# Performance work log

Measured on AMD Instinct MI355X. Metric: run time of the kernel, lower is better.

The kernel has to match this reference:

```python
import jax, jax.numpy as jnp
import numpy as np

B = 1048576


def _normalize_rotation_matrix(R):
    # Faithful to torch: U, S, V = svd(R); Rn = U @ V^T; flip whole U by sign(det); recompute.
    U, S, Vh = jnp.linalg.svd(R)  # R = U diag(S) Vh, so torch's V^T == Vh
    Rn = jnp.matmul(U, Vh)
    det = jnp.linalg.det(Rn)[:, None, None]
    sign = jnp.sign(det)
    U = U * sign
    return jnp.matmul(U, Vh)


def _quat_to_rotmat(q):
    # q: [B, 4] as (w, x, y, z); same element layout as the torch loop, vectorized.
    w, x, y, z = q[:, 0], q[:, 1], q[:, 2], q[:, 3]
    R = jnp.stack([
        1 - 2 * (y ** 2 + z ** 2), 2 * (x * y - w * z),     2 * (x * z + w * y),
        2 * (x * y + w * z),       1 - 2 * (x ** 2 + z ** 2), 2 * (y * z - w * x),
        2 * (x * z - w * y),       2 * (y * z + w * x),     1 - 2 * (x ** 2 + y ** 2),
    ], axis=-1)
    return R.reshape(-1, 3, 3)


def setup_inputs() -> dict:
    key = jax.random.key(0)
    k1, k2, k3 = jax.random.split(key, 3)
    pred_R = jax.random.normal(k1, (B, 3, 3), dtype=jnp.float32)
    pred_t = jax.random.normal(k2, (B, 1, 3), dtype=jnp.float32)
    gt_transform = jax.random.normal(k3, (B, 7), dtype=jnp.float32)
    return {"pred_R": pred_R, "pred_t": pred_t, "gt_transform": gt_transform}


def reference(pred_R, pred_t, gt_transform):
    gt_quat = gt_transform[:, :4]
    igt_t = gt_transform[:, 4:]
    igt_R = _quat_to_rotmat(gt_quat)              # [B,3,3]
    igt_R = _normalize_rotation_matrix(igt_R)
    pred_Rn = _normalize_rotation_matrix(pred_R)
    # matmul(pred_R^T, igt_R): [b,i,k] = sum_j pred_Rn[b,j,i] * igt_R[b,j,k]
    M = jnp.einsum('bji,bjk->bik', pred_Rn, igt_R)
    eye = jnp.eye(3, dtype=M.dtype)
    rot_loss = jnp.mean((M - eye) ** 2)
    t_loss = jnp.mean((pred_t - igt_t[:, None, :]) ** 2)
    return rot_loss + t_loss
```

## Files before the change

kernel.cpp:

```cpp
#include <hip/hip_runtime.h>


#define TILE 256
#define SCALED_ITERS 3
#define PLAIN_ITERS  1

__device__ __forceinline__ float se3_elem(const float* __restrict__ R,
                                          const float* __restrict__ Q,
                                          const float* __restrict__ T)
{
    float w  = Q[0], x = Q[1], y = Q[2], z = Q[3];

    float v2 = x*x + y*y + z*z;
    float c  = 1.0f - 2.0f*v2;
    float r2 = fmaxf(c*c + 4.0f*(w*w)*v2, 1e-30f);
    float rr = __builtin_amdgcn_rsqf(r2);
    float ga = c * rr;
    float gt_ = (1.0f - ga) * __builtin_amdgcn_rcpf(fmaxf(v2, 1e-37f));
    float gb = 2.0f * w * rr;

    float tx = gt_*x, ty = gt_*y, tz = gt_*z;
    float bx = gb*x,  by = gb*y,  bz = gb*z;

    float G0 = ga + tx*x,  G1 = tx*y - bz,   G2 = tx*z + by;
    float G3 = tx*y + bz,  G4 = ga + ty*y,   G5 = ty*z - bx;
    float G6 = tx*z - by,  G7 = ty*z + bx,   G8 = ga + tz*z;

    float X0 = R[0], X1 = R[1], X2 = R[2];
    float X3 = R[3], X4 = R[4], X5 = R[5];
    float X6 = R[6], X7 = R[7], X8 = R[8];

    float s = 1.0f;
#pragma unroll
    for (int it = 0; it < SCALED_ITERS + PLAIN_ITERS; ++it) {
        float C0 = X4*X8 - X5*X7;
        float C1 = X5*X6 - X3*X8;
        float C2 = X3*X7 - X4*X6;
        float C3 = X2*X7 - X1*X8;
        float C4 = X0*X8 - X2*X6;
        float C5 = X1*X6 - X0*X7;
        float C6 = X1*X5 - X2*X4;
        float C7 = X2*X3 - X0*X5;
        float C8 = X0*X4 - X1*X3;
        float det = X0*C0 + X1*C1 + X2*C2;
        if (it == 0) s = (det < 0.0f) ? -1.0f : 1.0f;
        float ka, kb;
        if (it < SCALED_ITERS) {
            float ad = fminf(fmaxf(fabsf(det), 1e-30f), 1e30f);
            float g  = __builtin_amdgcn_exp2f(0.33333333f * __builtin_amdgcn_logf(ad));
            ka = 0.5f * __builtin_amdgcn_rcpf(g);
            kb = 0.5f * g * __builtin_amdgcn_rcpf(det);
        } else {
            ka = 0.5f;
            kb = 0.5f * __builtin_amdgcn_rcpf(det);
        }
        if (it == SCALED_ITERS + PLAIN_ITERS - 1) { ka *= s; kb *= s; }
        X0 = ka*X0 + kb*C0;  X1 = ka*X1 + kb*C1;  X2 = ka*X2 + kb*C2;
        X3 = ka*X3 + kb*C3;  X4 = ka*X4 + kb*C4;  X5 = ka*X5 + kb*C5;
        X6 = ka*X6 + kb*C6;  X7 = ka*X7 + kb*C7;  X8 = ka*X8 + kb*C8;
    }

    float d0 = G0-X0, d1 = G1-X1, d2 = G2-X2;
    float d3 = G3-X3, d4 = G4-X4, d5 = G5-X5;
    float d6 = G6-X6, d7 = G7-X7, d8 = G8-X8;
    float rot = d0*d0 + d1*d1 + d2*d2
              + d3*d3 + d4*d4 + d5*d5
              + d6*d6 + d7*d7 + d8*d8;

    float e0 = T[0] - Q[4];
    float e1 = T[1] - Q[5];
    float e2 = T[2] - Q[6];
    float tl = e0*e0 + e1*e1 + e2*e2;

    return rot * (1.0f/9.0f) + tl * (1.0f/3.0f);
}

__device__ __forceinline__ float se3_block_partial(
    const float* __restrict__ pred_R,
    const float* __restrict__ pred_t,
    const float* __restrict__ gt,
    int B, float invB,
    float* ldsR, float* ldsQ, float* ldsT, float* wsums)
{
    const int tid  = threadIdx.x;
    const int base = blockIdx.x * TILE;
    int count = B - base;
    if (count > TILE) count = TILE;

    if (count == TILE) {
        const float4* sR = reinterpret_cast<const float4*>(pred_R) + (size_t)blockIdx.x * (TILE * 9 / 4);
        const float4* sQ = reinterpret_cast<const float4*>(gt)     + (size_t)blockIdx.x * (TILE * 7 / 4);
        const float4* sT = reinterpret_cast<const float4*>(pred_t) + (size_t)blockIdx.x * (TILE * 3 / 4);
        float4* dR = reinterpret_cast<float4*>(ldsR);
        float4* dQ = reinterpret_cast<float4*>(ldsQ);
        float4* dT = reinterpret_cast<float4*>(ldsT);

        float4 r0 = sR[tid];
        float4 r1 = sR[tid + 256];
        float4 r2; if (tid < 64)  r2 = sR[tid + 512];
        float4 q0 = sQ[tid];
        float4 q1; if (tid < 192) q1 = sQ[tid + 256];
        float4 t0; if (tid < 192) t0 = sT[tid];

        dR[tid]       = r0;
        dR[tid + 256] = r1;
        if (tid < 64)  dR[tid + 512] = r2;
        dQ[tid]       = q0;
        if (tid < 192) dQ[tid + 256] = q1;
        if (tid < 192) dT[tid]       = t0;
    } else {
        for (int i = tid; i < count * 9; i += 256) ldsR[i] = pred_R[(size_t)base * 9 + i];
        for (int i = tid; i < count * 7; i += 256) ldsQ[i] = gt[(size_t)base * 7 + i];
        for (int i = tid; i < count * 3; i += 256) ldsT[i] = pred_t[(size_t)base * 3 + i];
    }
    __syncthreads();

    float acc = 0.0f;
    if (tid < count)
        acc = se3_elem(&ldsR[9 * tid], &ldsQ[7 * tid], &ldsT[3 * tid]) * invB;

#pragma unroll
    for (int off = 32; off > 0; off >>= 1)
        acc += __shfl_down(acc, off, 64);

    int lane = tid & 63;
    int wid  = tid >> 6;
    if (lane == 0) wsums[wid] = acc;
    __syncthreads();
    return wsums[0] + wsums[1] + wsums[2] + wsums[3];
}

__global__ __launch_bounds__(256) void se3_partial_kernel(
    const float* __restrict__ pred_R,
    const float* __restrict__ pred_t,
    const float* __restrict__ gt,
    float* __restrict__ partials, int B, float invB)
{
    __shared__ __align__(16) float ldsR[TILE * 9];
    __shared__ __align__(16) float ldsQ[TILE * 7];
    __shared__ __align__(16) float ldsT[TILE * 3];
    __shared__ float wsums[4];

    float tot = se3_block_partial(pred_R, pred_t, gt, B, invB,
                                  ldsR, ldsQ, ldsT, wsums);
    if (threadIdx.x == 0)
        partials[blockIdx.x] = tot;
}

__global__ __launch_bounds__(256) void se3_atomic_kernel(
    const float* __restrict__ pred_R,
    const float* __restrict__ pred_t,
    const float* __restrict__ gt,
    float* __restrict__ out, int B, float invB)
{
    __shared__ __align__(16) float ldsR[TILE * 9];
    __shared__ __align__(16) float ldsQ[TILE * 7];
    __shared__ __align__(16) float ldsT[TILE * 3];
    __shared__ float wsums[4];

    float tot = se3_block_partial(pred_R, pred_t, gt, B, invB,
                                  ldsR, ldsQ, ldsT, wsums);
    if (threadIdx.x == 0)
        atomicAdd(out, tot);
}

__global__ __launch_bounds__(256) void se3_reduce_kernel(
    const float* __restrict__ partials, float* __restrict__ out, int n)
{
    float acc = 0.0f;
    for (int i = threadIdx.x; i < n; i += 256)
        acc += partials[i];

#pragma unroll
    for (int off = 32; off > 0; off >>= 1)
        acc += __shfl_down(acc, off, 64);

    __shared__ float wsums[4];
    int lane = threadIdx.x & 63;
    int wid  = threadIdx.x >> 6;
    if (lane == 0) wsums[wid] = acc;
    __syncthreads();
    if (threadIdx.x == 0)
        out[0] = wsums[0] + wsums[1] + wsums[2] + wsums[3];
}

extern "C" void kernel_launch(void* const* d_in, const int* in_sizes, int n_in,
                              void* d_out, int out_size, void* d_ws, size_t ws_size,
                              hipStream_t stream) {
    const float* pred_R = (const float*)d_in[0];
    const float* pred_t = (const float*)d_in[1];
    const float* gt     = (const float*)d_in[2];
    float* out = (float*)d_out;
    int B = in_sizes[0] / 9;

    const int block = 256;
    const int grid  = (B + TILE - 1) / TILE;

    if (d_ws != nullptr && ws_size >= (size_t)grid * sizeof(float)) {
        float* partials = (float*)d_ws;
        se3_partial_kernel<<<grid, block, 0, stream>>>(pred_R, pred_t, gt,
                                                       partials, B,
                                                       1.0f / (float)B);
        se3_reduce_kernel<<<1, block, 0, stream>>>(partials, out, grid);
    } else {
        hipMemsetAsync(out, 0, sizeof(float), stream);
        se3_atomic_kernel<<<grid, block, 0, stream>>>(pred_R, pred_t, gt,
                                                      out, B, 1.0f / (float)B);
    }
}
```

Baseline: 106.6 us.

## Process four tiles per block with double-buffered LDS and register prefetch

Each block of the partial kernel now handles four consecutive 256-element tiles. While it computes on one LDS buffer, it prefetches the next tile into registers and then stores it into the alternate buffer. The grid shrinks by four, so the partials array and the final reduction get smaller, and global load latency overlaps with the heavy per-element math. In exchange, LDS use per block doubles, which can lower occupancy, and extra barriers are added per tile.

```diff
diff --git a/kernel.cpp b/kernel.cpp
--- a/kernel.cpp
+++ b/kernel.cpp
@@ -2,6 +2,7 @@
 
 
 #define TILE 256
+#define TPB_TILES 4
 #define SCALED_ITERS 3
 #define PLAIN_ITERS  1
 
@@ -75,76 +76,114 @@
     return rot * (1.0f/9.0f) + tl * (1.0f/3.0f);
 }
 
-__device__ __forceinline__ float se3_block_partial(
-    const float* __restrict__ pred_R,
-    const float* __restrict__ pred_t,
-    const float* __restrict__ gt,
-    int B, float invB,
-    float* ldsR, float* ldsQ, float* ldsT, float* wsums)
-{
-    const int tid  = threadIdx.x;
-    const int base = blockIdx.x * TILE;
-    int count = B - base;
-    if (count > TILE) count = TILE;
-
-    if (count == TILE) {
-        const float4* sR = reinterpret_cast<const float4*>(pred_R) + (size_t)blockIdx.x * (TILE * 9 / 4);
-        const float4* sQ = reinterpret_cast<const float4*>(gt)     + (size_t)blockIdx.x * (TILE * 7 / 4);
-        const float4* sT = reinterpret_cast<const float4*>(pred_t) + (size_t)blockIdx.x * (TILE * 3 / 4);
-        float4* dR = reinterpret_cast<float4*>(ldsR);
-        float4* dQ = reinterpret_cast<float4*>(ldsQ);
-        float4* dT = reinterpret_cast<float4*>(ldsT);
-
-        float4 r0 = sR[tid];
-        float4 r1 = sR[tid + 256];
-        float4 r2; if (tid < 64)  r2 = sR[tid + 512];
-        float4 q0 = sQ[tid];
-        float4 q1; if (tid < 192) q1 = sQ[tid + 256];
-        float4 t0; if (tid < 192) t0 = sT[tid];
-
-        dR[tid]       = r0;
-        dR[tid + 256] = r1;
-        if (tid < 64)  dR[tid + 512] = r2;
-        dQ[tid]       = q0;
-        if (tid < 192) dQ[tid + 256] = q1;
-        if (tid < 192) dT[tid]       = t0;
-    } else {
-        for (int i = tid; i < count * 9; i += 256) ldsR[i] = pred_R[(size_t)base * 9 + i];
-        for (int i = tid; i < count * 7; i += 256) ldsQ[i] = gt[(size_t)base * 7 + i];
-        for (int i = tid; i < count * 3; i += 256) ldsT[i] = pred_t[(size_t)base * 3 + i];
-    }
-    __syncthreads();
-
-    float acc = 0.0f;
-    if (tid < count)
-        acc = se3_elem(&ldsR[9 * tid], &ldsQ[7 * tid], &ldsT[3 * tid]) * invB;
-
-#pragma unroll
-    for (int off = 32; off > 0; off >>= 1)
-        acc += __shfl_down(acc, off, 64);
-
-    int lane = tid & 63;
-    int wid  = tid >> 6;
-    if (lane == 0) wsums[wid] = acc;
-    __syncthreads();
-    return wsums[0] + wsums[1] + wsums[2] + wsums[3];
-}
-
 __global__ __launch_bounds__(256) void se3_partial_kernel(
     const float* __restrict__ pred_R,
     const float* __restrict__ pred_t,
     const float* __restrict__ gt,
     float* __restrict__ partials, int B, float invB)
 {
-    __shared__ __align__(16) float ldsR[TILE * 9];
-    __shared__ __align__(16) float ldsQ[TILE * 7];
-    __shared__ __align__(16) float ldsT[TILE * 3];
+    __shared__ __align__(16) float ldsR[2][TILE * 9];
+    __shared__ __align__(16) float ldsQ[2][TILE * 7];
+    __shared__ __align__(16) float ldsT[2][TILE * 3];
     __shared__ float wsums[4];
 
-    float tot = se3_block_partial(pred_R, pred_t, gt, B, invB,
-                                  ldsR, ldsQ, ldsT, wsums);
+    const int tid     = threadIdx.x;
+    const int ntiles  = (B + TILE - 1) / TILE;
+    const int tile0   = blockIdx.x * TPB_TILES;
+
+    float acc = 0.0f;
+
+    float4 r0, r1, r2, q0, q1, t0;
+
+    auto load_tile = [&](int tile) {
+        const float4* sR = reinterpret_cast<const float4*>(pred_R) + (size_t)tile * (TILE * 9 / 4);
+        const float4* sQ = reinterpret_cast<const float4*>(gt)     + (size_t)tile * (TILE * 7 / 4);
+        const float4* sT = reinterpret_cast<const float4*>(pred_t) + (size_t)tile * (TILE * 3 / 4);
+        r0 = sR[tid];
+        r1 = sR[tid + 256];
+        if (tid < 64)  r2 = sR[tid + 512];
+        q0 = sQ[tid];
+        if (tid < 192) { q1 = sQ[tid + 256]; t0 = sT[tid]; }
+    };
+    auto store_tile = [&](int buf) {
+        float4* dR = reinterpret_cast<float4*>(ldsR[buf]);
+        float4* dQ = reinterpret_cast<float4*>(ldsQ[buf]);
+        float4* dT = reinterpret_cast<float4*>(ldsT[buf]);
+        dR[tid]       = r0;
+        dR[tid + 256] = r1;
+        if (tid < 64)  dR[tid + 512] = r2;
+        dQ[tid]       = q0;
+        if (tid < 192) { dQ[tid + 256] = q1; dT[tid] = t0; }
+    };
+
+    const bool all_full = (tile0 + TPB_TILES) * TILE <= B;
+
+    if (all_full) {
+        load_tile(tile0);
+        store_tile(0);
+        __syncthreads();
+#pragma unroll
+        for (int lt = 0; lt < TPB_TILES; ++lt) {
+            if (lt + 1 < TPB_TILES) load_tile(tile0 + lt + 1);
+            const int buf = lt & 1;
+            acc += se3_elem(&ldsR[buf][9 * tid],
+                            &ldsQ[buf][7 * tid],
+                            &ldsT[buf][3 * tid]);
+            __syncthreads();
+            if (lt + 1 < TPB_TILES) {
+                store_tile((lt + 1) & 1);
+                __syncthreads();
+            }
+        }
+        acc *= invB;
+    } else {
+        for (int lt = 0; lt < TPB_TILES; ++lt) {
+            const int tile = tile0 + lt;
+            if (tile >= ntiles) break;
+            const int base  = tile * TILE;
+            int count = B - base;
+            if (count > TILE) count = TILE;
+            __syncthreads();
+            for (int i = tid; i < count * 9; i += 256) ldsR[0][i] = pred_R[(size_t)base * 9 + i];
+            for (int i = tid; i < count * 7; i += 256) ldsQ[0][i] = gt[(size_t)base * 7 + i];
+            for (int i = tid; i < count * 3; i += 256) ldsT[0][i] = pred_t[(size_t)base * 3 + i];
+            __syncthreads();
+            if (tid < count)
+                acc += se3_elem(&ldsR[0][9 * tid], &ldsQ[0][7 * tid], &ldsT[0][3 * tid]);
+        }
+        acc *= invB;
+    }
+
+#pragma unroll
+    for (int off = 32; off > 0; off >>= 1)
+        acc += __shfl_down(acc, off, 64);
+
+    int lane = tid & 63;
+    int wid  = tid >> 6;
+    if (lane == 0) wsums[wid] = acc;
+    __syncthreads();
+    if (tid == 0)
+        partials[blockIdx.x] = wsums[0] + wsums[1] + wsums[2] + wsums[3];
+}
+
+__global__ __launch_bounds__(256) void se3_reduce_kernel(
+    const float* __restrict__ partials, float* __restrict__ out, int n)
+{
+    float acc = 0.0f;
+    for (int i = threadIdx.x; i < n; i += 256)
+        acc += partials[i];
+
+#pragma unroll
+    for (int off = 32; off > 0; off >>= 1)
+        acc += __shfl_down(acc, off, 64);
+
+    __shared__ float wsums[4];
+    int lane = threadIdx.x & 63;
+    int wid  = threadIdx.x >> 6;
+    if (lane == 0) wsums[wid] = acc;
+    __syncthreads();
     if (threadIdx.x == 0)
-        partials[blockIdx.x] = tot;
+        out[0] = wsums[0] + wsums[1] + wsums[2] + wsums[3];
 }
 
 __global__ __launch_bounds__(256) void se3_atomic_kernel(
@@ -158,30 +197,30 @@
     __shared__ __align__(16) float ldsT[TILE * 3];
     __shared__ float wsums[4];
 
-    float tot = se3_block_partial(pred_R, pred_t, gt, B, invB,
-                                  ldsR, ldsQ, ldsT, wsums);
-    if (threadIdx.x == 0)
-        atomicAdd(out, tot);
-}
-
-__global__ __launch_bounds__(256) void se3_reduce_kernel(
-    const float* __restrict__ partials, float* __restrict__ out, int n)
-{
+    const int tid  = threadIdx.x;
+    const int base = blockIdx.x * TILE;
+    int count = B - base;
+    if (count > TILE) count = TILE;
+
+    for (int i = tid; i < count * 9; i += 256) ldsR[i] = pred_R[(size_t)base * 9 + i];
+    for (int i = tid; i < count * 7; i += 256) ldsQ[i] = gt[(size_t)base * 7 + i];
+    for (int i = tid; i < count * 3; i += 256) ldsT[i] = pred_t[(size_t)base * 3 + i];
+    __syncthreads();
+
     float acc = 0.0f;
-    for (int i = threadIdx.x; i < n; i += 256)
-        acc += partials[i];
+    if (tid < count)
+        acc = se3_elem(&ldsR[9 * tid], &ldsQ[7 * tid], &ldsT[3 * tid]) * invB;
 
 #pragma unroll
     for (int off = 32; off > 0; off >>= 1)
         acc += __shfl_down(acc, off, 64);
 
-    __shared__ float wsums[4];
-    int lane = threadIdx.x & 63;
-    int wid  = threadIdx.x >> 6;
+    int lane = tid & 63;
+    int wid  = tid >> 6;
     if (lane == 0) wsums[wid] = acc;
     __syncthreads();
-    if (threadIdx.x == 0)
-        out[0] = wsums[0] + wsums[1] + wsums[2] + wsums[3];
+    if (tid == 0)
+        atomicAdd(out, wsums[0] + wsums[1] + wsums[2] + wsums[3]);
 }
 
 extern "C" void kernel_launch(void* const* d_in, const int* in_sizes, int n_in,
@@ -193,8 +232,9 @@
     float* out = (float*)d_out;
     int B = in_sizes[0] / 9;
 
-    const int block = 256;
-    const int grid  = (B + TILE - 1) / TILE;
+    const int block  = 256;
+    const int ntiles = (B + TILE - 1) / TILE;
+    const int grid   = (ntiles + TPB_TILES - 1) / TPB_TILES;
 
     if (d_ws != nullptr && ws_size >= (size_t)grid * sizeof(float)) {
         float* partials = (float*)d_ws;
@@ -204,7 +244,7 @@
         se3_reduce_kernel<<<1, block, 0, stream>>>(partials, out, grid);
     } else {
         hipMemsetAsync(out, 0, sizeof(float), stream);
-        se3_atomic_kernel<<<grid, block, 0, stream>>>(pred_R, pred_t, gt,
-                                                      out, B, 1.0f / (float)B);
+        se3_atomic_kernel<<<ntiles, block, 0, stream>>>(pred_R, pred_t, gt,
+                                                        out, B, 1.0f / (float)B);
     }
 }
```

Result: no change. 106.5 us (-0.2%).
